# Optimization experiments

Measured on AMD Instinct MI355X. Metric: run time of the kernel, lower is better.

Reference implementation:

```python
import jax, jax.numpy as jnp
import numpy as np

DN = ('NCDHW', 'OIDHW', 'NCDHW')


def conv3(x, w):
    # 3x3x3 'same' conv (submanifold conv on a dense volume == padded dense conv)
    return jax.lax.conv_general_dilated(x, w, (1, 1, 1), [(1, 1)] * 3, dimension_numbers=DN)


def conv1(x, w):
    # 1x1x1 conv
    return jax.lax.conv_general_dilated(x, w, (1, 1, 1), 'VALID', dimension_numbers=DN)


def avg_pool(x, ksz):
    s = jax.lax.reduce_window(x, 0.0, jax.lax.add, (1, 1) + ksz, (1, 1) + ksz, 'VALID')
    return s / float(np.prod(ksz))


def setup_inputs() -> dict:
    key = jax.random.key(0)
    ks = jax.random.split(key, 14)
    B, C, D, H, W = 1, 64, 48, 64, 128
    n_dense = 5  # nconvs - 1

    def he(k, shape, fan):
        return jax.random.normal(k, shape, jnp.float32) * np.sqrt(2.0 / fan).astype(np.float32)

    return {
        'fvl': jax.random.normal(ks[0], (B, C, D, H, W), jnp.float32),
        'w_a1': he(ks[1], (C, C, 3, 3, 3), 27 * C),
        'w_a2': he(ks[2], (C, C, 3, 3, 3), 27 * C),
        'w_nin': he(ks[3], (C, C, 1, 1, 1), C),
        'w1s': he(ks[4], (n_dense, C, C, 1, 1, 1), C),
        'w2s': he(ks[5], (n_dense, C, C, 1, 1, 1), C),
        'wp0': he(ks[6], (C, C, 1, 1, 1), C),
        'wp1': he(ks[7], (C, C, 1, 1, 1), C),
        'wp2': he(ks[8], (C, C, 1, 1, 1), C),
        'wp3': he(ks[9], (C, C, 1, 1, 1), C),
        'wc1': he(ks[10], (C, C, 3, 3, 3), 27 * C),
        'wc2': he(ks[11], (1, C, 3, 3, 3), 27 * 1),
        'bc': jnp.zeros((1,), jnp.float32),
    }


def reference(fvl, w_a1, w_a2, w_nin, w1s, w2s, wp0, wp1, wp2, wp3, wc1, wc2, bc):
    # --- Conv3dBlock_sparse: (conv3 -> conv3) + NIN(1x1), summed (no relu) ---
    x = conv3(conv3(fvl, w_a1), w_a2) + conv1(fvl, w_nin)
    # --- (nconvs-1) dense 1x1x1 residual blocks: relu(conv1(x) + conv2(conv1(x))) ---
    for i in range(w1s.shape[0]):
        x1 = conv1(x, w1s[i])
        x2 = conv1(x1, w2s[i])
        x = jax.nn.relu(x1 + x2)
    # --- PSP-style multi-scale pool pyramid ---
    B, C, d, h, w = x.shape
    pool_ws = [wp0, wp1, wp2, wp3]
    out_sum = x
    for i, ps in enumerate(np.linspace(1, min(d, h, w) // 2, 4, dtype=int)):
        ksz = (int(d / ps), int(h / ps), int(w / ps))
        o = avg_pool(x, ksz)
        o = conv1(o, pool_ws[i])
        o = jax.image.resize(o, (B, C, d, h, w), method='trilinear')  # align_corners=False semantics
        out_sum = out_sum + 0.25 * o
    x = jax.nn.relu(out_sum / 2.0)
    # --- classify head (eval path, up=False): conv3 -> relu -> conv3(+bias) ---
    c = conv3(jax.nn.relu(conv3(x, wc1)), wc2) + bc.reshape(1, -1, 1, 1, 1)
    return (x, jnp.squeeze(c, 1))
```

## Files before the change

kernel.cpp:

```cpp
#include <hip/hip_runtime.h>
#include <math.h>

#define DD 48
#define HH 64
#define WW 128
#define VOL (DD*HH*WW)
#define PW 130
#define PROWS (DD*HH)
#define PVOL (PROWS*PW)
#define PVBYTES ((long)PVOL*64*2)
#define GUARD 16640L
#define NC 64

typedef __attribute__((ext_vector_type(8))) short bf16x8;
typedef __attribute__((ext_vector_type(4))) float f32x4;
typedef __attribute__((ext_vector_type(4))) unsigned int u32x4v;
typedef __attribute__((ext_vector_type(2))) unsigned int u32x2v;

__device__ __forceinline__ float bflo(unsigned int u){
    union { unsigned int i; float f; } x; x.i = u<<16; return x.f; }
__device__ __forceinline__ float bfhi(unsigned int u){
    union { unsigned int i; float f; } x; x.i = u & 0xffff0000u; return x.f; }
__device__ __forceinline__ float bf2f(unsigned short u){
    union { unsigned int i; float f; } x; x.i = ((unsigned int)u)<<16; return x.f; }
__device__ __forceinline__ unsigned short f2bf(float f){
    union { float f; unsigned int i; } x; x.f = f;
    unsigned int i = x.i;
    return (unsigned short)((i + 0x7fffu + ((i>>16)&1u)) >> 16);
}

__device__ __forceinline__ void gload16(const void* g, void* l){
    __builtin_amdgcn_global_load_lds(
        (const __attribute__((address_space(1))) void*)g,
        (__attribute__((address_space(3))) void*)l, 16, 0, 0);
}


__global__ void k_wprep3(const float* __restrict__ src, unsigned short* __restrict__ dst){
    int idx = blockIdx.x*256 + threadIdx.x;
    if (idx >= 27*64*64) return;
    int ci = idx & 63; int t = idx >> 6; int co = t & 63; int k = t >> 6;
    dst[idx] = f2bf(src[(co*64+ci)*27 + k]);
}

__global__ void k_wprep1(const float* __restrict__ src, unsigned short* __restrict__ dst){
    int idx = blockIdx.x*256 + threadIdx.x;
    if (idx >= 4096) return;
    dst[idx] = f2bf(src[idx]);
}

__global__ void k_wprep2(const float* __restrict__ src, unsigned short* __restrict__ dst){
    int idx = blockIdx.x*256 + threadIdx.x;
    if (idx >= 32*64) return;
    int co = idx & 63; int row = idx >> 6;
    float v = (row < 27) ? src[co*27 + row] : 0.f;
    dst[row*64 + co] = f2bf(v);
}

__global__ void k_fuse_res(const float* __restrict__ w1, const float* __restrict__ w2,
                           unsigned short* __restrict__ mt){
    int idx = blockIdx.x*256 + threadIdx.x;
    if (idx >= 5*4096) return;
    int i = idx >> 12; int r = idx & 4095;
    int co = r >> 6; int ci = r & 63;
    const float* W1 = w1 + i*4096;
    const float* W2 = w2 + i*4096;
    float m = W1[co*64+ci];
    for (int k=0;k<64;++k) m += W2[co*64+k]*W1[k*64+ci];
    mt[idx] = f2bf(m);
}

__global__ void k_transpose1(const float* __restrict__ src, float* __restrict__ dst){
    int idx = blockIdx.x*256 + threadIdx.x;
    if (idx >= 4096) return;
    int ci = idx >> 6; int co = idx & 63;
    dst[idx] = src[co*64+ci];
}

__global__ __launch_bounds__(256) void k_zeropad(unsigned short* __restrict__ pv0,
                                                 unsigned short* __restrict__ pv1){
    int idx = blockIdx.x*256 + threadIdx.x;
    int seg = idx >> 3, part = idx & 7;
    int vol = seg / 6144; int r2 = seg - vol*6144;
    int row = r2 >> 1; int col = (r2 & 1) ? 129 : 0;
    long boff = ((long)row*130 + col)*128 + part*16;
    u32x4v z = {0,0,0,0};
    char* base = (char*)(vol ? pv1 : pv0);
    *(u32x4v*)(base + boff) = z;
}

__global__ __launch_bounds__(256) void k_tobf16v(const float* __restrict__ src,
                                                 unsigned short* __restrict__ dst){
    __shared__ unsigned short lds[64*66];
    int tid = threadIdx.x;
    long vbase = (long)blockIdx.x*64;
    int d = (int)(vbase >> 13);
    int h = (int)((vbase >> 7) & 63);
    int w0 = (int)(vbase & 127);
    long pbase = ((long)(d*64+h)*PW + w0 + 1);
    int v = tid & 63;
    int cg = tid >> 6;
#pragma unroll
    for (int k=0;k<16;++k){
        int ci = cg*16 + k;
        lds[v*66 + ci] = f2bf(src[(long)ci*VOL + vbase + v]);
    }
    __syncthreads();
#pragma unroll
    for (int it=0; it<2; ++it){
        int chunk = it*256 + tid;
        int vv = chunk >> 3, gp = chunk & 7;
        const unsigned short* s = lds + vv*66 + gp*8;
        unsigned int w0_ = (unsigned)s[0] | ((unsigned)s[1]<<16);
        unsigned int w1_ = (unsigned)s[2] | ((unsigned)s[3]<<16);
        unsigned int w2_ = (unsigned)s[4] | ((unsigned)s[5]<<16);
        unsigned int w3_ = (unsigned)s[6] | ((unsigned)s[7]<<16);
        u32x4v q = {w0_,w1_,w2_,w3_};
        *(u32x4v*)(dst + (pbase+vv)*64 + gp*8) = q;
    }
}

template<bool AUX, bool RELU>
__global__ __launch_bounds__(256,2) void k_conv3m(
    const unsigned short* __restrict__ in, const unsigned short* __restrict__ wt,
    const unsigned short* __restrict__ aux, const unsigned short* __restrict__ auxw,
    unsigned short* __restrict__ out)
{
    __shared__ __align__(16) char sA[36864];
    __shared__ __align__(16) char sB[33280];

    const int tid  = threadIdx.x;
    const int lane = tid & 63;
    const int wave = tid >> 6;
    const int ll = lane & 15;
    const int kg = lane >> 4;
    const int bid = blockIdx.x;
    const int wid = ((bid & 7) * 192) + (bid >> 3);
    const int vbr = wid*256;
    const int d  = vbr >> 13;
    const int h0 = (vbr >> 7) & 63;
    const int my_h  = h0 + (wave >> 1);
    const int my_w0 = (wave & 1) * 64;
    const long pvb = (long)(d*64 + my_h)*PW + my_w0 + 1;

    const char* inb = (const char*)in;
    const char* wtb = (const char*)wt;

    f32x4 acc[4][4];
#pragma unroll
    for (int a=0;a<4;++a)
#pragma unroll
        for (int b=0;b<4;++b) acc[a][b] = (f32x4){0.f,0.f,0.f,0.f};

#pragma unroll
    for (int kd=0; kd<3; ++kd){
        const int dd = d + kd - 1;
        if ((unsigned)dd >= 48u) continue;
        const long rowstart = ((long)(dd*64 + h0 - 1)) * 130;
#pragma unroll
        for (int khalf=0; khalf<2; ++khalf){
            __syncthreads();
#pragma unroll
            for (int rnd=0; rnd<9; ++rnd){
                int j = rnd*4096 + tid*16;
                int q = j ^ (((j>>7)&3)<<4);
                const char* src = wtb + (long)(kd*9 + (q>>12))*8192
                                      + (long)((q>>6)&63)*128 + khalf*64 + (q&63);
                gload16(src, sA + j);
            }
#pragma unroll
            for (int rnd=0; rnd<8; ++rnd){
                int j = rnd*4096 + tid*16;
                int q = j ^ (((j>>7)&3)<<4);
                const char* src = inb + (rowstart + (q>>6))*128 + khalf*64 + (q&63);
                gload16(src, sB + j);
            }
            if (tid < 32){
                int j = 32768 + tid*16;
                int q = j ^ (((j>>7)&3)<<4);
                const char* src = inb + (rowstart + (q>>6))*128 + khalf*64 + (q&63);
                gload16(src, sB + j);
            }
            __syncthreads();
#pragma unroll
            for (int kh=0; kh<3; ++kh){
                const int hh = my_h + kh - 1;
                if ((unsigned)hh >= 64u) continue;
                const int rr = (wave>>1) + kh;
#pragma unroll
                for (int kw=0; kw<3; ++kw){
                    const int tap_rel = kh*3 + kw;
                    bf16x8 Af[4], Bf[4];
#pragma unroll
                    for (int t=0;t<4;++t){
                        int qa = tap_rel*4096 + (t*16+ll)*64 + kg*16;
                        Af[t] = *(const bf16x8*)(sA + (qa ^ (((qa>>7)&3)<<4)));
                    }
#pragma unroll
                    for (int vt=0; vt<4; ++vt){
                        int vrel = rr*130 + my_w0 + vt*16 + ll + kw;
                        int qb = vrel*64 + kg*16;
                        Bf[vt] = *(const bf16x8*)(sB + (qb ^ (((qb>>7)&3)<<4)));
                    }
#pragma unroll
                    for (int vt=0; vt<4; ++vt)
#pragma unroll
                        for (int t=0; t<4; ++t)
                            acc[t][vt] = __builtin_amdgcn_mfma_f32_16x16x32_bf16(Af[t], Bf[vt], acc[t][vt], 0,0,0);
                }
            }
        }
    }

    if (AUX){
        bf16x8 Aa[2][4], Ba[2][4];
#pragma unroll
        for (int half=0; half<2; ++half){
            const int ko = half*32 + kg*8;
#pragma unroll
            for (int t=0;t<4;++t)
                Aa[half][t] = *(const bf16x8*)(auxw + (t*16+ll)*64 + ko);
#pragma unroll
            for (int vt=0; vt<4; ++vt)
                Ba[half][vt] = *(const bf16x8*)(aux + (pvb + vt*16 + ll)*64 + ko);
        }
#pragma unroll
        for (int half=0; half<2; ++half)
#pragma unroll
            for (int vt=0; vt<4; ++vt)
#pragma unroll
                for (int t=0;t<4;++t)
                    acc[t][vt] = __builtin_amdgcn_mfma_f32_16x16x32_bf16(Aa[half][t], Ba[half][vt], acc[t][vt], 0,0,0);
    }

#pragma unroll
    for (int vt=0; vt<4; ++vt){
        unsigned short* op = out + (pvb + vt*16 + ll)*64 + kg*4;
#pragma unroll
        for (int t=0;t<4;++t){
            float r0 = acc[t][vt][0], r1 = acc[t][vt][1], r2 = acc[t][vt][2], r3 = acc[t][vt][3];
            if (RELU){ r0=fmaxf(r0,0.f); r1=fmaxf(r1,0.f); r2=fmaxf(r2,0.f); r3=fmaxf(r3,0.f); }
            unsigned int lo = (unsigned)f2bf(r0) | ((unsigned)f2bf(r1)<<16);
            unsigned int hi = (unsigned)f2bf(r2) | ((unsigned)f2bf(r3)<<16);
            u32x2v q = {lo, hi};
            *(u32x2v*)(op + t*16) = q;
        }
    }
}

__global__ __launch_bounds__(256,3) void k_chain(const unsigned short* __restrict__ in,
        const unsigned short* __restrict__ Mt, unsigned short* __restrict__ out){
    __shared__ __align__(16) char sX[4][8192];
    const int lane = threadIdx.x & 63;
    const int wave = threadIdx.x >> 6;
    const int ll = lane & 15;
    const int kg = lane >> 4;
    const long vb = (long)blockIdx.x*256 + wave*64;
    char* myL = sX[wave];

    bf16x8 B[2][4];
#pragma unroll
    for (int half=0; half<2; ++half){
        const int ko = half*32 + kg*8;
#pragma unroll
        for (int vt=0; vt<4; ++vt)
            B[half][vt] = *(const bf16x8*)(in + (vb+vt*16+ll)*64 + ko);
    }

#pragma unroll
    for (int s=0; s<5; ++s){
        const unsigned short* wt = Mt + s*4096;
        bf16x8 A[2][4];
#pragma unroll
        for (int half=0; half<2; ++half){
            const int ko = half*32 + kg*8;
#pragma unroll
            for (int t=0;t<4;++t)
                A[half][t] = *(const bf16x8*)(wt + (t*16+ll)*64 + ko);
        }
        f32x4 acc[4][4];
#pragma unroll
        for (int a=0;a<4;++a)
#pragma unroll
            for (int b=0;b<4;++b) acc[a][b] = (f32x4){0.f,0.f,0.f,0.f};
#pragma unroll
        for (int half=0; half<2; ++half)
#pragma unroll
            for (int vt=0; vt<4; ++vt)
#pragma unroll
                for (int t=0;t<4;++t)
                    acc[t][vt] = __builtin_amdgcn_mfma_f32_16x16x32_bf16(A[half][t], B[half][vt], acc[t][vt], 0,0,0);

        if (s < 4){
#pragma unroll
            for (int vt=0; vt<4; ++vt){
                const int row = vt*16 + ll;
                const int sw = (row & 7) << 4;
#pragma unroll
                for (int t=0;t<4;++t){
                    float r0 = fmaxf(acc[t][vt][0],0.f), r1 = fmaxf(acc[t][vt][1],0.f);
                    float r2 = fmaxf(acc[t][vt][2],0.f), r3 = fmaxf(acc[t][vt][3],0.f);
                    unsigned int lo = (unsigned)f2bf(r0) | ((unsigned)f2bf(r1)<<16);
                    unsigned int hi = (unsigned)f2bf(r2) | ((unsigned)f2bf(r3)<<16);
                    u32x2v q = {lo, hi};
                    int colb = kg*8 + t*32;
                    *(u32x2v*)(myL + row*128 + (colb ^ sw)) = q;
                }
            }
#pragma unroll
            for (int half=0; half<2; ++half){
#pragma unroll
                for (int vt=0; vt<4; ++vt){
                    const int row = vt*16 + ll;
                    const int sw = (row & 7) << 4;
                    int colb = half*64 + kg*16;
                    B[half][vt] = *(const bf16x8*)(myL + row*128 + (colb ^ sw));
                }
            }
        } else {
#pragma unroll
            for (int vt=0; vt<4; ++vt){
                unsigned short* op = out + (vb+vt*16+ll)*64 + kg*4;
#pragma unroll
                for (int t=0;t<4;++t){
                    float r0 = fmaxf(acc[t][vt][0],0.f), r1 = fmaxf(acc[t][vt][1],0.f);
                    float r2 = fmaxf(acc[t][vt][2],0.f), r3 = fmaxf(acc[t][vt][3],0.f);
                    unsigned int lo = (unsigned)f2bf(r0) | ((unsigned)f2bf(r1)<<16);
                    unsigned int hi = (unsigned)f2bf(r2) | ((unsigned)f2bf(r3)<<16);
                    u32x2v q = {lo, hi};
                    *(u32x2v*)(op + t*16) = q;
                }
            }
        }
    }
}

__global__ __launch_bounds__(256) void k_headt(const unsigned short* __restrict__ in,
        const unsigned short* __restrict__ wt2, float* __restrict__ t){
    const int lane = threadIdx.x & 63;
    const int wave = threadIdx.x >> 6;
    const int ll = lane & 15;
    const int kg = lane >> 4;
    const long vb = (long)blockIdx.x*256 + wave*64;

    f32x4 acc[2][4];
#pragma unroll
    for (int a=0;a<2;++a)
#pragma unroll
        for (int b=0;b<4;++b) acc[a][b] = (f32x4){0.f,0.f,0.f,0.f};

#pragma unroll
    for (int khalf=0; khalf<2; ++khalf){
        const int ko = khalf*32 + kg*8;
        bf16x8 afr[2];
#pragma unroll
        for (int tl=0;tl<2;++tl)
            afr[tl] = *(const bf16x8*)(wt2 + (tl*16+ll)*64 + ko);
#pragma unroll
        for (int vt=0; vt<4; ++vt){
            bf16x8 bfr = *(const bf16x8*)(in + (vb+vt*16+ll)*64 + ko);
#pragma unroll
            for (int tl=0;tl<2;++tl)
                acc[tl][vt] = __builtin_amdgcn_mfma_f32_16x16x32_bf16(afr[tl], bfr, acc[tl][vt], 0,0,0);
        }
    }
#pragma unroll
    for (int vt=0; vt<4; ++vt){
        long vx = vb + vt*16 + ll;
#pragma unroll
        for (int tl=0;tl<2;++tl){
#pragma unroll
            for (int r=0;r<4;++r){
                int tap = tl*16 + kg*4 + r;
                if (tap < 27) t[(long)tap*PVOL + vx] = acc[tl][vt][r];
            }
        }
    }
}

__global__ __launch_bounds__(256) void k_heads(const float* __restrict__ t,
        const float* __restrict__ bias, float* __restrict__ out){
    int v = blockIdx.x*256 + threadIdx.x;
    int ww = v & 127; int h = (v>>7)&63; int d = v>>13;
    long p = (long)(d*64+h)*PW + ww + 1;
    float s = bias[0];
#pragma unroll
    for (int kd=0;kd<3;++kd){
#pragma unroll
      for (int kh=0;kh<3;++kh){
#pragma unroll
        for (int kw=0;kw<3;++kw){
            const int tap = (kd*3+kh)*3+kw;
            const long dvp = (long)((kd-1)*64 + (kh-1))*PW + (kw-1);
            bool ok = ((unsigned)(d+kd-1)<48u) && ((unsigned)(h+kh-1)<64u);
            long va = ok ? (p + dvp) : p;
            float x = t[(long)tap*PVOL + va];
            s += ok ? x : 0.f;
        }
      }
    }
    out[v] = s;
}

__global__ __launch_bounds__(256) void k_pool3(const unsigned short* __restrict__ in,
                                               float* __restrict__ S3){
    __shared__ float sm[32*68];
    int tid = threadIdx.x;
    int cg = tid & 7, part = tid >> 3;
    int cell = blockIdx.x;
    int Z = cell >> 8, Y = (cell >> 4) & 15, X = cell & 15;
    float a[8];
#pragma unroll
    for (int j=0;j<8;++j) a[j]=0.f;
#pragma unroll
    for (int j=0;j<3;++j){
        int i = part*3 + j;
        int di = i >> 5, rem = i & 31, hi = rem >> 3, wi = rem & 7;
        long p = ((long)((3*Z+di)*64 + 4*Y+hi))*PW + 8*X+wi + 1;
        u32x4v q = *(const u32x4v*)(in + p*64 + cg*8);
#pragma unroll
        for (int e=0;e<4;++e){ a[e*2] += bflo(q[e]); a[e*2+1] += bfhi(q[e]); }
    }
#pragma unroll
    for (int j=0;j<8;++j) sm[part*68 + cg*8 + j] = a[j];
    __syncthreads();
    if (tid < 64){
        float s=0.f;
        for (int r=0;r<32;++r) s += sm[r*68 + tid];
        S3[tid*4096 + cell] = s;
    }
}

__global__ __launch_bounds__(256) void k_pool2(const float* __restrict__ S3,
                                               float* __restrict__ P2){
    int idx = blockIdx.x*256 + threadIdx.x;
    int cell = idx & 511; int c = idx >> 9;
    int z = cell >> 6, y = (cell >> 3) & 7, x = cell & 7;
    const float* b = S3 + c*4096;
    float s = 0.f;
#pragma unroll
    for (int a2=0;a2<2;++a2)
#pragma unroll
        for (int b2=0;b2<2;++b2)
#pragma unroll
            for (int e=0;e<2;++e)
                s += b[((2*z+a2)<<8) + ((2*y+b2)<<4) + (2*x+e)];
    P2[c*512 + cell] = s;
}

__global__ void k_gcm(const float* __restrict__ S3, const float* __restrict__ wp0,
                      float* __restrict__ gc){
    __shared__ float sm[4][64];
    __shared__ float sg[64];
    int tid = threadIdx.x;
    int c = tid & 63, part = tid >> 6;
    float s = 0.f;
    const float* row = S3 + c*4096 + part*1024;
    for (int i=0;i<1024;i+=4){
        f32x4 q = *(const f32x4*)(row + i);
        s += q[0]+q[1]+q[2]+q[3];
    }
    sm[part][c] = s;
    __syncthreads();
    if (tid < 64){
        sg[tid] = (sm[0][tid]+sm[1][tid]+sm[2][tid]+sm[3][tid]) * (1.0f/(float)VOL);
    }
    __syncthreads();
    if (tid < 64){
        float g=0.f;
        for (int ci=0;ci<64;++ci) g += wp0[tid*64+ci]*sg[ci];
        gc[tid] = g;
    }
}

__global__ __launch_bounds__(256) void k_pool4(const unsigned short* __restrict__ in,
                                               float* __restrict__ P4){
    __shared__ float sm[32*68];
    int tid = threadIdx.x;
    int cg = tid & 7, part = (tid >> 3) & 3, slot = tid >> 5;
    int cell = blockIdx.x*8 + slot;
    int z = cell / 800; int rem = cell - z*800; int y = rem / 25; int x = rem - y*25;
    int a2 = part >> 1, b2 = part & 1;
    float a[8];
#pragma unroll
    for (int j=0;j<8;++j) a[j]=0.f;
#pragma unroll
    for (int e=0;e<5;++e){
        long p = ((long)((2*z+a2)*64 + 2*y+b2))*PW + 5*x+e + 1;
        u32x4v q = *(const u32x4v*)(in + p*64 + cg*8);
#pragma unroll
        for (int k=0;k<4;++k){ a[k*2] += bflo(q[k]); a[k*2+1] += bfhi(q[k]); }
    }
#pragma unroll
    for (int j=0;j<8;++j) sm[(slot*4+part)*68 + cg*8 + j] = a[j];
    __syncthreads();
#pragma unroll
    for (int r=0;r<2;++r){
        int o = r*256 + tid;
        int c = o >> 3, s = o & 7;
        float v = sm[(s*4+0)*68 + c] + sm[(s*4+1)*68 + c]
                + sm[(s*4+2)*68 + c] + sm[(s*4+3)*68 + c];
        P4[(long)c*19200 + blockIdx.x*8 + s] = v;
    }
}

__global__ void k_conv1(const float* __restrict__ in, const float* __restrict__ wt,
                        float* __restrict__ out, int vol, float scale){
    int v = blockIdx.x*256 + threadIdx.x;
    if (v >= vol) return;
    float acc[64];
#pragma unroll
    for (int i=0;i<64;++i) acc[i]=0.f;
    for (int ci=0; ci<64; ++ci){
        float xv = in[ci*vol + v];
        const float* wr = wt + ci*64;
#pragma unroll
        for (int co=0; co<64; ++co) acc[co] = fmaf(wr[co], xv, acc[co]);
    }
    float* op = out + (long)v*64;
#pragma unroll
    for (int q=0;q<16;++q){
        f32x4 t = {acc[q*4]*scale, acc[q*4+1]*scale, acc[q*4+2]*scale, acc[q*4+3]*scale};
        *(f32x4*)(op + q*4) = t;
    }
}

__device__ __forceinline__ void tri_setup(int d,int h,int w,int gd,int gh,int gw,
                                          int* o, float* wt){
    float fz = (d+0.5f)*((float)gd/(float)DD) - 0.5f;
    float fy = (h+0.5f)*((float)gh/(float)HH) - 0.5f;
    float fx = (w+0.5f)*((float)gw/(float)WW) - 0.5f;
    float z0f = floorf(fz), y0f = floorf(fy), x0f = floorf(fx);
    float tz = fz - z0f, ty = fy - y0f, tx = fx - x0f;
    int z0 = (int)z0f, y0 = (int)y0f, x0 = (int)x0f;
    int z1 = z0+1, y1 = y0+1, x1 = x0+1;
    z0 = min(max(z0,0),gd-1); z1 = min(max(z1,0),gd-1);
    y0 = min(max(y0,0),gh-1); y1 = min(max(y1,0),gh-1);
    x0 = min(max(x0,0),gw-1); x1 = min(max(x1,0),gw-1);
    o[0] = (z0*gh+y0)*gw+x0; wt[0] = (1-tz)*(1-ty)*(1-tx);
    o[1] = (z0*gh+y0)*gw+x1; wt[1] = (1-tz)*(1-ty)*tx;
    o[2] = (z0*gh+y1)*gw+x0; wt[2] = (1-tz)*ty*(1-tx);
    o[3] = (z0*gh+y1)*gw+x1; wt[3] = (1-tz)*ty*tx;
    o[4] = (z1*gh+y0)*gw+x0; wt[4] = tz*(1-ty)*(1-tx);
    o[5] = (z1*gh+y0)*gw+x1; wt[5] = tz*(1-ty)*tx;
    o[6] = (z1*gh+y1)*gw+x0; wt[6] = tz*ty*(1-tx);
    o[7] = (z1*gh+y1)*gw+x1; wt[7] = tz*ty*tx;
}

__global__ __launch_bounds__(256) void k_combine(
        const unsigned short* __restrict__ xc, const float* __restrict__ gc,
        const float* __restrict__ p2, const float* __restrict__ p3,
        const float* __restrict__ p4, float* __restrict__ xout,
        unsigned short* __restrict__ xv){
    int tid = threadIdx.x;
    const int bid = blockIdx.x;
    const int wid = ((bid & 7) * 192) + (bid >> 3);
    long v = (long)wid*256 + tid;
    int w = v & 127; int h = (v>>7)&63; int d = v>>13;
    long p = (long)(d*64+h)*PW + w + 1;
    int o2[8], o3[8], o4[8];
    float w2_[8], w3_[8], w4_[8];
    tri_setup(d,h,w, 8,8,8,    o2, w2_);
    tri_setup(d,h,w, 16,16,16, o3, w3_);
    tri_setup(d,h,w, 24,32,25, o4, w4_);
#pragma unroll
    for (int half=0; half<2; ++half){
        float res[32];
#pragma unroll
        for (int j=0;j<32;++j) res[j] = gc[half*32+j];
#pragma unroll
        for (int t=0;t<8;++t){
            const float* b2 = p2 + (long)o2[t]*64 + half*32;
#pragma unroll
            for (int q=0;q<8;++q){
                f32x4 x4 = *(const f32x4*)(b2 + q*4);
                res[q*4+0] = fmaf(w2_[t], x4[0], res[q*4+0]);
                res[q*4+1] = fmaf(w2_[t], x4[1], res[q*4+1]);
                res[q*4+2] = fmaf(w2_[t], x4[2], res[q*4+2]);
                res[q*4+3] = fmaf(w2_[t], x4[3], res[q*4+3]);
            }
        }
#pragma unroll
        for (int t=0;t<8;++t){
            const float* b3 = p3 + (long)o3[t]*64 + half*32;
#pragma unroll
            for (int q=0;q<8;++q){
                f32x4 x4 = *(const f32x4*)(b3 + q*4);
                res[q*4+0] = fmaf(w3_[t], x4[0], res[q*4+0]);
                res[q*4+1] = fmaf(w3_[t], x4[1], res[q*4+1]);
                res[q*4+2] = fmaf(w3_[t], x4[2], res[q*4+2]);
                res[q*4+3] = fmaf(w3_[t], x4[3], res[q*4+3]);
            }
        }
#pragma unroll
        for (int t=0;t<8;++t){
            const float* b4 = p4 + (long)o4[t]*64 + half*32;
#pragma unroll
            for (int q=0;q<8;++q){
                f32x4 x4 = *(const f32x4*)(b4 + q*4);
                res[q*4+0] = fmaf(w4_[t], x4[0], res[q*4+0]);
                res[q*4+1] = fmaf(w4_[t], x4[1], res[q*4+1]);
                res[q*4+2] = fmaf(w4_[t], x4[2], res[q*4+2]);
                res[q*4+3] = fmaf(w4_[t], x4[3], res[q*4+3]);
            }
        }
        const u32x4v* xq = (const u32x4v*)(xc + p*64 + half*32);
#pragma unroll
        for (int q=0;q<4;++q){
            u32x4v qv = xq[q];
            unsigned int pk[4];
#pragma unroll
            for (int e=0;e<4;++e){
                int j = q*8 + e*2;
                float r0 = fmaxf((bflo(qv[e]) + 0.25f*res[j])*0.5f, 0.f);
                float r1 = fmaxf((bfhi(qv[e]) + 0.25f*res[j+1])*0.5f, 0.f);
                __builtin_nontemporal_store(r0, &xout[(long)(half*32+j)*VOL + v]);
                __builtin_nontemporal_store(r1, &xout[(long)(half*32+j+1)*VOL + v]);
                pk[e] = (unsigned)f2bf(r0) | ((unsigned)f2bf(r1)<<16);
            }
            u32x4v pq = {pk[0],pk[1],pk[2],pk[3]};
            *(u32x4v*)(xv + p*64 + half*32 + q*8) = pq;
        }
    }
}

constexpr long RPV = GUARD + PVBYTES + GUARD;
constexpr long OFF_PV0R = 0;
constexpr long OFF_PV1R = RPV;
constexpr long OFF_WA1 = 2*RPV;
constexpr long OFF_WA2 = OFF_WA1 + 221184;
constexpr long OFF_WC1 = OFF_WA2 + 221184;
constexpr long OFF_NIN = OFF_WC1 + 221184;
constexpr long OFF_MT  = OFF_NIN + 8192;
constexpr long OFF_WT2 = OFF_MT + 40960;
constexpr long OFF_WPT = OFF_WT2 + 4096;
constexpr long OFF_GC  = OFF_WPT + 49152;
constexpr long OFF_P2  = OFF_GC + 256;
constexpr long OFF_P2C = OFF_P2 + 131072;
constexpr long OFF_S3  = OFF_P2C + 131072;
constexpr long OFF_P3C = OFF_S3 + 1048576;
constexpr long OFF_P4  = OFF_P3C + 1048576;
constexpr long OFF_P4C = OFF_P4 + 4915200;

extern "C" void kernel_launch(void* const* d_in, const int* in_sizes, int n_in,
                              void* d_out, int out_size, void* d_ws, size_t ws_size,
                              hipStream_t stream) {
    const float* fvl  = (const float*)d_in[0];
    const float* w_a1 = (const float*)d_in[1];
    const float* w_a2 = (const float*)d_in[2];
    const float* wnin = (const float*)d_in[3];
    const float* w1s  = (const float*)d_in[4];
    const float* w2s  = (const float*)d_in[5];
    const float* wp0  = (const float*)d_in[6];
    const float* wp1  = (const float*)d_in[7];
    const float* wp2  = (const float*)d_in[8];
    const float* wp3  = (const float*)d_in[9];
    const float* wc1  = (const float*)d_in[10];
    const float* wc2  = (const float*)d_in[11];
    const float* bc   = (const float*)d_in[12];

    char* ws = (char*)d_ws;
    unsigned short* PV0  = (unsigned short*)(ws + OFF_PV0R + GUARD);
    unsigned short* PV1  = (unsigned short*)(ws + OFF_PV1R + GUARD);
    unsigned short* wa1t = (unsigned short*)(ws + OFF_WA1);
    unsigned short* wa2t = (unsigned short*)(ws + OFF_WA2);
    unsigned short* wc1t = (unsigned short*)(ws + OFF_WC1);
    unsigned short* nint = (unsigned short*)(ws + OFF_NIN);
    unsigned short* Mt   = (unsigned short*)(ws + OFF_MT);
    unsigned short* wt2  = (unsigned short*)(ws + OFF_WT2);
    float* wpt  = (float*)(ws + OFF_WPT);
    float* gc   = (float*)(ws + OFF_GC);
    float* p2   = (float*)(ws + OFF_P2);
    float* p2c  = (float*)(ws + OFF_P2C);
    float* S3   = (float*)(ws + OFF_S3);
    float* p3c  = (float*)(ws + OFF_P3C);
    float* p4   = (float*)(ws + OFF_P4);
    float* p4c  = (float*)(ws + OFF_P4C);

    float* Xout = (float*)d_out;
    float* Cout = Xout + (long)NC*VOL;
    float* Tbuf = (float*)PV0;

    const int GBR = VOL/256;
    const int GBP = PVOL/256;

    k_zeropad<<<384,256,0,stream>>>(PV0, PV1);

    k_wprep3<<<(27*64*64+255)/256,256,0,stream>>>(w_a1, wa1t);
    k_wprep3<<<(27*64*64+255)/256,256,0,stream>>>(w_a2, wa2t);
    k_wprep3<<<(27*64*64+255)/256,256,0,stream>>>(wc1, wc1t);
    k_wprep1<<<16,256,0,stream>>>(wnin, nint);
    k_wprep2<<<8,256,0,stream>>>(wc2, wt2);
    k_fuse_res<<<80,256,0,stream>>>(w1s, w2s, Mt);
    k_transpose1<<<16,256,0,stream>>>(wp1, wpt + 0*4096);
    k_transpose1<<<16,256,0,stream>>>(wp2, wpt + 1*4096);
    k_transpose1<<<16,256,0,stream>>>(wp3, wpt + 2*4096);
    k_tobf16v<<<VOL/64,256,0,stream>>>(fvl, PV0);

    k_conv3m<false,false><<<GBR,256,0,stream>>>(PV0, wa1t, nullptr, nullptr, PV1);
    k_conv3m<true,false><<<GBR,256,0,stream>>>(PV1, wa2t, PV0, nint, PV0);

    k_chain<<<GBP,256,0,stream>>>(PV0, Mt, PV1);

    k_pool3<<<4096,256,0,stream>>>(PV1, S3);
    k_gcm<<<1,256,0,stream>>>(S3, wp0, gc);
    k_pool2<<<128,256,0,stream>>>(S3, p2);
    k_pool4<<<2400,256,0,stream>>>(PV1, p4);
    k_conv1<<<2,256,0,stream>>>(p2, wpt + 0*4096, p2c, 512,   1.0f/768.0f);
    k_conv1<<<16,256,0,stream>>>(S3, wpt + 1*4096, p3c, 4096, 1.0f/96.0f);
    k_conv1<<<75,256,0,stream>>>(p4, wpt + 2*4096, p4c, 19200, 1.0f/20.0f);

    k_combine<<<GBR,256,0,stream>>>(PV1, gc, p2c, p3c, p4c, Xout, PV0);

    k_conv3m<false,true><<<GBR,256,0,stream>>>(PV0, wc1t, nullptr, nullptr, PV1);
    k_headt<<<GBP,256,0,stream>>>(PV1, wt2, Tbuf);
    k_heads<<<GBR,256,0,stream>>>(Tbuf, bc, Cout);
}
```

Baseline: 615.4 us.

## Merge weight prep kernels, store head taps in bf16, split combine channel halves

Nine small weight-preparation launches become a single kernel that dispatches on block index, cutting launch overhead. The head's 27-tap intermediate buffer is stored as bf16 instead of fp32, halving its write and read traffic at some precision cost. The combine kernel now assigns each channel half to a separate thread and doubles the grid, which raises parallelism and lowers per-thread register pressure, but the trilinear setup is computed twice.

```diff
diff --git a/kernel.cpp b/kernel.cpp
--- a/kernel.cpp
+++ b/kernel.cpp
@@ -35,46 +35,52 @@
         (__attribute__((address_space(3))) void*)l, 16, 0, 0);
 }
 
-
-__global__ void k_wprep3(const float* __restrict__ src, unsigned short* __restrict__ dst){
-    int idx = blockIdx.x*256 + threadIdx.x;
-    if (idx >= 27*64*64) return;
-    int ci = idx & 63; int t = idx >> 6; int co = t & 63; int k = t >> 6;
-    dst[idx] = f2bf(src[(co*64+ci)*27 + k]);
-}
-
-__global__ void k_wprep1(const float* __restrict__ src, unsigned short* __restrict__ dst){
-    int idx = blockIdx.x*256 + threadIdx.x;
-    if (idx >= 4096) return;
-    dst[idx] = f2bf(src[idx]);
-}
-
-__global__ void k_wprep2(const float* __restrict__ src, unsigned short* __restrict__ dst){
-    int idx = blockIdx.x*256 + threadIdx.x;
-    if (idx >= 32*64) return;
-    int co = idx & 63; int row = idx >> 6;
-    float v = (row < 27) ? src[co*27 + row] : 0.f;
-    dst[row*64 + co] = f2bf(v);
-}
-
-__global__ void k_fuse_res(const float* __restrict__ w1, const float* __restrict__ w2,
-                           unsigned short* __restrict__ mt){
-    int idx = blockIdx.x*256 + threadIdx.x;
-    if (idx >= 5*4096) return;
-    int i = idx >> 12; int r = idx & 4095;
-    int co = r >> 6; int ci = r & 63;
-    const float* W1 = w1 + i*4096;
-    const float* W2 = w2 + i*4096;
-    float m = W1[co*64+ci];
-    for (int k=0;k<64;++k) m += W2[co*64+k]*W1[k*64+ci];
-    mt[idx] = f2bf(m);
-}
-
-__global__ void k_transpose1(const float* __restrict__ src, float* __restrict__ dst){
-    int idx = blockIdx.x*256 + threadIdx.x;
-    if (idx >= 4096) return;
-    int ci = idx >> 6; int co = idx & 63;
-    dst[idx] = src[co*64+ci];
+__global__ void k_prep_all(
+    const float* __restrict__ w_a1, const float* __restrict__ w_a2,
+    const float* __restrict__ wc1,  const float* __restrict__ wnin,
+    const float* __restrict__ wc2,  const float* __restrict__ w1s,
+    const float* __restrict__ w2s,  const float* __restrict__ wp1,
+    const float* __restrict__ wp2,  const float* __restrict__ wp3,
+    unsigned short* __restrict__ wa1t, unsigned short* __restrict__ wa2t,
+    unsigned short* __restrict__ wc1t, unsigned short* __restrict__ nint,
+    unsigned short* __restrict__ wt2,  unsigned short* __restrict__ Mt,
+    float* __restrict__ wpt)
+{
+    int b = blockIdx.x, tid = threadIdx.x;
+    if (b < 1296){
+        int which = b/432, bb = b - which*432;
+        int idx = bb*256 + tid;
+        if (idx < 27*64*64){
+            const float* src = which==0 ? w_a1 : (which==1 ? w_a2 : wc1);
+            unsigned short* dst = which==0 ? wa1t : (which==1 ? wa2t : wc1t);
+            int ci = idx & 63; int t = idx >> 6; int co = t & 63; int k = t >> 6;
+            dst[idx] = f2bf(src[(co*64+ci)*27 + k]);
+        }
+    } else if (b < 1376){
+        int idx = (b-1296)*256 + tid;
+        int i = idx >> 12; int r = idx & 4095;
+        int co = r >> 6; int ci = r & 63;
+        const float* W1 = w1s + i*4096;
+        const float* W2 = w2s + i*4096;
+        float m = W1[co*64+ci];
+        for (int k=0;k<64;++k) m += W2[co*64+k]*W1[k*64+ci];
+        Mt[idx] = f2bf(m);
+    } else if (b < 1392){
+        int idx = (b-1376)*256 + tid;
+        nint[idx] = f2bf(wnin[idx]);
+    } else if (b < 1400){
+        int idx = (b-1392)*256 + tid;
+        int co = idx & 63; int row = idx >> 6;
+        float v = (row < 27) ? wc2[co*27 + row] : 0.f;
+        wt2[row*64 + co] = f2bf(v);
+    } else {
+        int bb = b - 1400;
+        int which = bb/16;
+        int idx = (bb - which*16)*256 + tid;
+        const float* src = which==0 ? wp1 : (which==1 ? wp2 : wp3);
+        int ci = idx >> 6; int co = idx & 63;
+        wpt[which*4096 + idx] = src[co*64+ci];
+    }
 }
 
 __global__ __launch_bounds__(256) void k_zeropad(unsigned short* __restrict__ pv0,
@@ -336,7 +342,7 @@
 }
 
 __global__ __launch_bounds__(256) void k_headt(const unsigned short* __restrict__ in,
-        const unsigned short* __restrict__ wt2, float* __restrict__ t){
+        const unsigned short* __restrict__ wt2, unsigned short* __restrict__ t){
     const int lane = threadIdx.x & 63;
     const int wave = threadIdx.x >> 6;
     const int ll = lane & 15;
@@ -372,13 +378,13 @@
 #pragma unroll
             for (int r=0;r<4;++r){
                 int tap = tl*16 + kg*4 + r;
-                if (tap < 27) t[(long)tap*PVOL + vx] = acc[tl][vt][r];
+                if (tap < 27) t[(long)tap*PVOL + vx] = f2bf(acc[tl][vt][r]);
             }
         }
     }
 }
 
-__global__ __launch_bounds__(256) void k_heads(const float* __restrict__ t,
+__global__ __launch_bounds__(256) void k_heads(const unsigned short* __restrict__ t,
         const float* __restrict__ bias, float* __restrict__ out){
     int v = blockIdx.x*256 + threadIdx.x;
     int ww = v & 127; int h = (v>>7)&63; int d = v>>13;
@@ -394,7 +400,7 @@
             const long dvp = (long)((kd-1)*64 + (kh-1))*PW + (kw-1);
             bool ok = ((unsigned)(d+kd-1)<48u) && ((unsigned)(h+kh-1)<64u);
             long va = ok ? (p + dvp) : p;
-            float x = t[(long)tap*PVOL + va];
+            float x = bf2f(t[(long)tap*PVOL + va]);
             s += ok ? x : 0.f;
         }
       }
@@ -554,8 +560,9 @@
         unsigned short* __restrict__ xv){
     int tid = threadIdx.x;
     const int bid = blockIdx.x;
-    const int wid = ((bid & 7) * 192) + (bid >> 3);
-    long v = (long)wid*256 + tid;
+    const int wid = ((bid & 7) * 384) + (bid >> 3);
+    const int half = tid >> 7;
+    long v = (long)wid*128 + (tid & 127);
     int w = v & 127; int h = (v>>7)&63; int d = v>>13;
     long p = (long)(d*64+h)*PW + w + 1;
     int o2[8], o3[8], o4[8];
@@ -563,64 +570,62 @@
     tri_setup(d,h,w, 8,8,8,    o2, w2_);
     tri_setup(d,h,w, 16,16,16, o3, w3_);
     tri_setup(d,h,w, 24,32,25, o4, w4_);
-#pragma unroll
-    for (int half=0; half<2; ++half){
-        float res[32];
-#pragma unroll
-        for (int j=0;j<32;++j) res[j] = gc[half*32+j];
-#pragma unroll
-        for (int t=0;t<8;++t){
-            const float* b2 = p2 + (long)o2[t]*64 + half*32;
-#pragma unroll
-            for (int q=0;q<8;++q){
-                f32x4 x4 = *(const f32x4*)(b2 + q*4);
-                res[q*4+0] = fmaf(w2_[t], x4[0], res[q*4+0]);
-                res[q*4+1] = fmaf(w2_[t], x4[1], res[q*4+1]);
-                res[q*4+2] = fmaf(w2_[t], x4[2], res[q*4+2]);
-                res[q*4+3] = fmaf(w2_[t], x4[3], res[q*4+3]);
-            }
-        }
-#pragma unroll
-        for (int t=0;t<8;++t){
-            const float* b3 = p3 + (long)o3[t]*64 + half*32;
-#pragma unroll
-            for (int q=0;q<8;++q){
-                f32x4 x4 = *(const f32x4*)(b3 + q*4);
-                res[q*4+0] = fmaf(w3_[t], x4[0], res[q*4+0]);
-                res[q*4+1] = fmaf(w3_[t], x4[1], res[q*4+1]);
-                res[q*4+2] = fmaf(w3_[t], x4[2], res[q*4+2]);
-                res[q*4+3] = fmaf(w3_[t], x4[3], res[q*4+3]);
-            }
-        }
-#pragma unroll
-        for (int t=0;t<8;++t){
-            const float* b4 = p4 + (long)o4[t]*64 + half*32;
-#pragma unroll
-            for (int q=0;q<8;++q){
-                f32x4 x4 = *(const f32x4*)(b4 + q*4);
-                res[q*4+0] = fmaf(w4_[t], x4[0], res[q*4+0]);
-                res[q*4+1] = fmaf(w4_[t], x4[1], res[q*4+1]);
-                res[q*4+2] = fmaf(w4_[t], x4[2], res[q*4+2]);
-                res[q*4+3] = fmaf(w4_[t], x4[3], res[q*4+3]);
-            }
-        }
-        const u32x4v* xq = (const u32x4v*)(xc + p*64 + half*32);
-#pragma unroll
-        for (int q=0;q<4;++q){
-            u32x4v qv = xq[q];
-            unsigned int pk[4];
-#pragma unroll
-            for (int e=0;e<4;++e){
-                int j = q*8 + e*2;
-                float r0 = fmaxf((bflo(qv[e]) + 0.25f*res[j])*0.5f, 0.f);
-                float r1 = fmaxf((bfhi(qv[e]) + 0.25f*res[j+1])*0.5f, 0.f);
-                __builtin_nontemporal_store(r0, &xout[(long)(half*32+j)*VOL + v]);
-                __builtin_nontemporal_store(r1, &xout[(long)(half*32+j+1)*VOL + v]);
-                pk[e] = (unsigned)f2bf(r0) | ((unsigned)f2bf(r1)<<16);
-            }
-            u32x4v pq = {pk[0],pk[1],pk[2],pk[3]};
-            *(u32x4v*)(xv + p*64 + half*32 + q*8) = pq;
-        }
+
+    float res[32];
+#pragma unroll
+    for (int j=0;j<32;++j) res[j] = gc[half*32+j];
+#pragma unroll
+    for (int t=0;t<8;++t){
+        const float* b2 = p2 + (long)o2[t]*64 + half*32;
+#pragma unroll
+        for (int q=0;q<8;++q){
+            f32x4 x4 = *(const f32x4*)(b2 + q*4);
+            res[q*4+0] = fmaf(w2_[t], x4[0], res[q*4+0]);
+            res[q*4+1] = fmaf(w2_[t], x4[1], res[q*4+1]);
+            res[q*4+2] = fmaf(w2_[t], x4[2], res[q*4+2]);
+            res[q*4+3] = fmaf(w2_[t], x4[3], res[q*4+3]);
+        }
+    }
+#pragma unroll
+    for (int t=0;t<8;++t){
+        const float* b3 = p3 + (long)o3[t]*64 + half*32;
+#pragma unroll
+        for (int q=0;q<8;++q){
+            f32x4 x4 = *(const f32x4*)(b3 + q*4);
+            res[q*4+0] = fmaf(w3_[t], x4[0], res[q*4+0]);
+            res[q*4+1] = fmaf(w3_[t], x4[1], res[q*4+1]);
+            res[q*4+2] = fmaf(w3_[t], x4[2], res[q*4+2]);
+            res[q*4+3] = fmaf(w3_[t], x4[3], res[q*4+3]);
+        }
+    }
+#pragma unroll
+    for (int t=0;t<8;++t){
+        const float* b4 = p4 + (long)o4[t]*64 + half*32;
+#pragma unroll
+        for (int q=0;q<8;++q){
+            f32x4 x4 = *(const f32x4*)(b4 + q*4);
+            res[q*4+0] = fmaf(w4_[t], x4[0], res[q*4+0]);
+            res[q*4+1] = fmaf(w4_[t], x4[1], res[q*4+1]);
+            res[q*4+2] = fmaf(w4_[t], x4[2], res[q*4+2]);
+            res[q*4+3] = fmaf(w4_[t], x4[3], res[q*4+3]);
+        }
+    }
+    const u32x4v* xq = (const u32x4v*)(xc + p*64 + half*32);
+#pragma unroll
+    for (int q=0;q<4;++q){
+        u32x4v qv = xq[q];
+        unsigned int pk[4];
+#pragma unroll
+        for (int e=0;e<4;++e){
+            int j = q*8 + e*2;
+            float r0 = fmaxf((bflo(qv[e]) + 0.25f*res[j])*0.5f, 0.f);
+            float r1 = fmaxf((bfhi(qv[e]) + 0.25f*res[j+1])*0.5f, 0.f);
+            __builtin_nontemporal_store(r0, &xout[(long)(half*32+j)*VOL + v]);
+            __builtin_nontemporal_store(r1, &xout[(long)(half*32+j+1)*VOL + v]);
+            pk[e] = (unsigned)f2bf(r0) | ((unsigned)f2bf(r1)<<16);
+        }
+        u32x4v pq = {pk[0],pk[1],pk[2],pk[3]};
+        *(u32x4v*)(xv + p*64 + half*32 + q*8) = pq;
     }
 }
 
@@ -679,22 +684,16 @@
 
     float* Xout = (float*)d_out;
     float* Cout = Xout + (long)NC*VOL;
-    float* Tbuf = (float*)PV0;
+    unsigned short* Tbuf = (unsigned short*)PV0;
 
     const int GBR = VOL/256;
     const int GBP = PVOL/256;
 
     k_zeropad<<<384,256,0,stream>>>(PV0, PV1);
 
-    k_wprep3<<<(27*64*64+255)/256,256,0,stream>>>(w_a1, wa1t);
-    k_wprep3<<<(27*64*64+255)/256,256,0,stream>>>(w_a2, wa2t);
-    k_wprep3<<<(27*64*64+255)/256,256,0,stream>>>(wc1, wc1t);
-    k_wprep1<<<16,256,0,stream>>>(wnin, nint);
-    k_wprep2<<<8,256,0,stream>>>(wc2, wt2);
-    k_fuse_res<<<80,256,0,stream>>>(w1s, w2s, Mt);
-    k_transpose1<<<16,256,0,stream>>>(wp1, wpt + 0*4096);
-    k_transpose1<<<16,256,0,stream>>>(wp2, wpt + 1*4096);
-    k_transpose1<<<16,256,0,stream>>>(wp3, wpt + 2*4096);
+    k_prep_all<<<1448,256,0,stream>>>(w_a1, w_a2, wc1, wnin, wc2, w1s, w2s,
+                                      wp1, wp2, wp3,
+                                      wa1t, wa2t, wc1t, nint, wt2, Mt, wpt);
     k_tobf16v<<<VOL/64,256,0,stream>>>(fvl, PV0);
 
     k_conv3m<false,false><<<GBR,256,0,stream>>>(PV0, wa1t, nullptr, nullptr, PV1);
@@ -710,7 +709,7 @@
     k_conv1<<<16,256,0,stream>>>(S3, wpt + 1*4096, p3c, 4096, 1.0f/96.0f);
     k_conv1<<<75,256,0,stream>>>(p4, wpt + 2*4096, p4c, 19200, 1.0f/20.0f);
 
-    k_combine<<<GBR,256,0,stream>>>(PV1, gc, p2c, p3c, p4c, Xout, PV0);
+    k_combine<<<3072,256,0,stream>>>(PV1, gc, p2c, p3c, p4c, Xout, PV0);
 
     k_conv3m<false,true><<<GBR,256,0,stream>>>(PV0, wc1t, nullptr, nullptr, PV1);
     k_headt<<<GBP,256,0,stream>>>(PV1, wt2, Tbuf);
```

Measured after the change: 600.3 us. 2.4% less time.
